# Performance work log

Measured on AMD Instinct MI355X. Metric: run time of the kernel, lower is better.

Reference implementation:

```python
import jax, jax.numpy as jnp
import numpy as np

N = 100_000
E = 1_600_000
F_IN = 128
HEADS = 8
OUT_H = 8   # per-head channels, concat -> 64
N_CLS = 40
K_HOPS = 10  # truncation order of heat-kernel Taylor series
NEG_SLOPE = 0.2
T_INIT = 5.0


def setup_inputs() -> dict:
    key = jax.random.key(0)
    ks = jax.random.split(key, 10)
    x = jax.random.normal(ks[0], (N, F_IN), jnp.float32)
    edge_index = jax.random.randint(ks[1], (2, E), 0, N, jnp.int32)
    t = jnp.full((F_IN,), T_INIT, jnp.float32)  # per-channel learnable diffusion time
    W1 = jax.random.normal(ks[2], (F_IN, HEADS * OUT_H), jnp.float32) / np.sqrt(F_IN).astype(np.float32)
    a_src1 = jax.random.normal(ks[3], (HEADS, OUT_H), jnp.float32) * 0.1
    a_dst1 = jax.random.normal(ks[4], (HEADS, OUT_H), jnp.float32) * 0.1
    b1 = jnp.zeros((HEADS * OUT_H,), jnp.float32)
    W2 = jax.random.normal(ks[5], (HEADS * OUT_H, N_CLS), jnp.float32) / np.sqrt(HEADS * OUT_H).astype(np.float32)
    a_src2 = jax.random.normal(ks[6], (1, N_CLS), jnp.float32) * 0.1
    a_dst2 = jax.random.normal(ks[7], (1, N_CLS), jnp.float32) * 0.1
    b2 = jnp.zeros((N_CLS,), jnp.float32)
    return {"x": x, "edge_index": edge_index, "t": t, "W1": W1, "a_src1": a_src1,
            "a_dst1": a_dst1, "b1": b1, "W2": W2, "a_src2": a_src2, "a_dst2": a_dst2, "b2": b2}


def _add_self_loops(edge_index, n):
    loop = jnp.arange(n, dtype=edge_index.dtype)
    return jnp.concatenate([edge_index, jnp.stack([loop, loop])], axis=1)


def _diffusion(x, src, dst, t, n):
    # heat kernel: exp(-t) * sum_k t^k/k! * A_hat^k x, per-channel t
    deg = jax.ops.segment_sum(jnp.ones_like(src, jnp.float32), dst, num_segments=n)
    dinv = jnp.where(deg > 0, jax.lax.rsqrt(jnp.maximum(deg, 1.0)), 0.0)
    norm = dinv[src] * dinv[dst]  # [E+N]

    def prop(h):
        return jax.ops.segment_sum(norm[:, None] * h[src], dst, num_segments=n)

    coef0 = jnp.exp(-t)  # [F]

    def step(carry, k):
        h, coef, acc = carry
        h = prop(h)
        coef = coef * t / k
        return (h, coef, acc + coef * h), None

    (_, _, out), _ = jax.lax.scan(step, (x, coef0, coef0 * x),
                                  jnp.arange(1, K_HOPS + 1, dtype=jnp.float32))
    return out


def _gat_layer(x, src, dst, W, a_s, a_d, b, heads, out_ch, concat, n):
    h = (x @ W).reshape(n, heads, out_ch)                  # [N,H,C]
    al_s = jnp.einsum('nhc,hc->nh', h, a_s)                # src attn logits
    al_d = jnp.einsum('nhc,hc->nh', h, a_d)
    e = jax.nn.leaky_relu(al_s[src] + al_d[dst], NEG_SLOPE)  # [E+N, H]
    emax = jax.ops.segment_max(e, dst, num_segments=n)       # stable softmax per target node
    ex = jnp.exp(e - emax[dst])
    denom = jax.ops.segment_sum(ex, dst, num_segments=n)
    alpha = ex / jnp.maximum(denom[dst], 1e-16)               # [E+N, H]
    out = jax.ops.segment_sum(alpha[:, :, None] * h[src], dst, num_segments=n)  # [N,H,C]
    out = out.reshape(n, heads * out_ch) if concat else out.mean(axis=1)
    return out + b


def reference(x, edge_index, t, W1, a_src1, a_dst1, b1, W2, a_src2, a_dst2, b2):
    n = x.shape[0]
    ei = _add_self_loops(edge_index, n)
    src, dst = ei[0], ei[1]
    h = _diffusion(x, src, dst, t, n)
    h = _gat_layer(h, src, dst, W1, a_src1, a_dst1, b1, HEADS, OUT_H, True, n)
    h = jax.nn.elu(h)
    h = _gat_layer(h, src, dst, W2, a_src2, a_dst2, b2, 1, N_CLS, False, n)
    return jax.nn.log_softmax(h, axis=1)
```

## Files before the change

kernel.cpp:

```cpp
#include <hip/hip_runtime.h>
#include <hip/hip_bf16.h>


static __device__ __forceinline__ unsigned pack_bf16x2(float a, float b) {
    __hip_bfloat162 p(__float2bfloat16(a), __float2bfloat16(b));
    return *reinterpret_cast<unsigned*>(&p);
}

__global__ void init_node_kernel(int* deg, int* cursor, int n) {
    int i = blockIdx.x * 256 + threadIdx.x;
    if (i < n) { deg[i] = 1; cursor[i] = 0; }
}

__global__ void edge_deg_kernel(const int* __restrict__ dst, int* deg, int E) {
    int e = blockIdx.x * 256 + threadIdx.x;
    if (e < E) atomicAdd(&deg[dst[e]], 1);
}

__global__ void alloc_kernel(const int* __restrict__ deg, float* dinv,
                             int* row_off, int* gcount, int n) {
    int i = blockIdx.x * 256 + threadIdx.x;
    if (i >= n) return;
    int dg = deg[i];
    dinv[i] = rsqrtf((float)dg);
    row_off[i] = atomicAdd(gcount, dg);
}

__global__ void scatter_kernel(const int* __restrict__ ei, const int* __restrict__ row_off,
                               int* cursor, const float* __restrict__ dinv,
                               int2* csr_pair, int E, int n) {
    int e = blockIdx.x * 256 + threadIdx.x;
    if (e >= E + n) return;
    int s, d;
    if (e < E) { s = ei[e]; d = ei[E + e]; } else { s = e - E; d = s; }
    int pos = atomicAdd(&cursor[d], 1);
    int slot = row_off[d] + pos;
    csr_pair[slot] = make_int2(s, __float_as_int(dinv[s] * dinv[d]));
}

__global__ void coef_kernel(const float* __restrict__ t, float* coefs) {
    int c = threadIdx.x;
    float tc = t[c];
    float v = expf(-tc);
    coefs[c] = v;
    for (int k = 1; k <= 10; ++k) { v *= tc / (float)k; coefs[k * 128 + c] = v; }
}

__global__ void init_diff_kernel(const float4* __restrict__ x4, const float* __restrict__ coefs,
                                 uint2* __restrict__ h, float4* __restrict__ acc4, int total4) {
    int i = blockIdx.x * 256 + threadIdx.x;
    if (i >= total4) return;
    float4 xv = x4[i];
    h[i] = make_uint2(pack_bf16x2(xv.x, xv.y), pack_bf16x2(xv.z, xv.w));
    const float4 c = *(const float4*)&coefs[(i & 31) * 4];
    acc4[i] = make_float4(c.x * xv.x, c.y * xv.y, c.z * xv.z, c.w * xv.w);
}

__global__ void hop_kernel(const int* __restrict__ row_off, const int* __restrict__ deg,
                           const int2* __restrict__ csr_pair,
                           const unsigned* __restrict__ h, unsigned* __restrict__ h_next,
                           float2* __restrict__ acc2, const float2* __restrict__ coefk2,
                           int n, int write_h) {
    int wid = (blockIdx.x << 2) + (threadIdx.x >> 6);
    int lane = threadIdx.x & 63;
    if (wid >= n) return;
    int off = row_off[wid];
    int cnt = deg[wid];
    float2 a0 = {0.f, 0.f}, a1 = {0.f, 0.f}, a2 = {0.f, 0.f}, a3 = {0.f, 0.f};
    for (int base = 0; base < cnt; base += 64) {
        int nb = min(64, cnt - base);
        int2 p = {0, 0};
        if (lane < nb) p = csr_pair[off + base + lane];
        int tt = 0;
        for (; tt + 3 < nb; tt += 4) {
            int s0 = __builtin_amdgcn_readlane(p.x, tt);
            int s1 = __builtin_amdgcn_readlane(p.x, tt + 1);
            int s2 = __builtin_amdgcn_readlane(p.x, tt + 2);
            int s3 = __builtin_amdgcn_readlane(p.x, tt + 3);
            float w0 = __int_as_float(__builtin_amdgcn_readlane(p.y, tt));
            float w1 = __int_as_float(__builtin_amdgcn_readlane(p.y, tt + 1));
            float w2 = __int_as_float(__builtin_amdgcn_readlane(p.y, tt + 2));
            float w3 = __int_as_float(__builtin_amdgcn_readlane(p.y, tt + 3));
            unsigned u0 = h[(size_t)s0 * 64 + lane];
            unsigned u1 = h[(size_t)s1 * 64 + lane];
            unsigned u2 = h[(size_t)s2 * 64 + lane];
            unsigned u3 = h[(size_t)s3 * 64 + lane];
            a0.x = fmaf(w0, __uint_as_float(u0 << 16), a0.x);
            a0.y = fmaf(w0, __uint_as_float(u0 & 0xffff0000u), a0.y);
            a1.x = fmaf(w1, __uint_as_float(u1 << 16), a1.x);
            a1.y = fmaf(w1, __uint_as_float(u1 & 0xffff0000u), a1.y);
            a2.x = fmaf(w2, __uint_as_float(u2 << 16), a2.x);
            a2.y = fmaf(w2, __uint_as_float(u2 & 0xffff0000u), a2.y);
            a3.x = fmaf(w3, __uint_as_float(u3 << 16), a3.x);
            a3.y = fmaf(w3, __uint_as_float(u3 & 0xffff0000u), a3.y);
        }
        for (; tt < nb; ++tt) {
            int s = __builtin_amdgcn_readlane(p.x, tt);
            float w = __int_as_float(__builtin_amdgcn_readlane(p.y, tt));
            unsigned u = h[(size_t)s * 64 + lane];
            a0.x = fmaf(w, __uint_as_float(u << 16), a0.x);
            a0.y = fmaf(w, __uint_as_float(u & 0xffff0000u), a0.y);
        }
    }
    float2 s;
    s.x = (a0.x + a1.x) + (a2.x + a3.x);
    s.y = (a0.y + a1.y) + (a2.y + a3.y);
    size_t o = (size_t)wid * 64 + lane;
    if (write_h) h_next[o] = pack_bf16x2(s.x, s.y);
    float2 c = coefk2[lane];
    float2 av = acc2[o];
    av.x = fmaf(c.x, s.x, av.x);
    av.y = fmaf(c.y, s.y, av.y);
    acc2[o] = av;
}

__global__ __launch_bounds__(256) void gemm1_kernel(
    const float* __restrict__ acc, const float* __restrict__ W1,
    const float* __restrict__ a_s, const float* __restrict__ a_d,
    float* __restrict__ h1, float* __restrict__ als, float* __restrict__ ald, int n) {
    __shared__ float Wl[128 * 64];
    __shared__ float Al[4][16 * 128];
    for (int i = threadIdx.x; i < 128 * 64; i += 256) Wl[i] = W1[i];
    int w = threadIdx.x >> 6;
    int lane = threadIdx.x & 63;
    int node0 = (blockIdx.x * 4 + w) * 16;
    const float4* accv4 = (const float4*)acc;
    float4* Av4 = (float4*)Al[w];
#pragma unroll
    for (int i = 0; i < 8; ++i) {
        int f4 = i * 64 + lane;
        int g4 = node0 * 32 + f4;
        float4 v = (g4 < n * 32) ? accv4[g4] : make_float4(0.f, 0.f, 0.f, 0.f);
        Av4[f4] = v;
    }
    __syncthreads();
    float sums[16];
#pragma unroll
    for (int nd = 0; nd < 16; ++nd) sums[nd] = 0.f;
#pragma unroll 1
    for (int kc = 0; kc < 16; ++kc) {
        float wr[8];
#pragma unroll
        for (int i = 0; i < 8; ++i) wr[i] = Wl[(kc * 8 + i) * 64 + lane];
#pragma unroll
        for (int nd = 0; nd < 16; ++nd) {
            float4 a = *(const float4*)&Al[w][nd * 128 + kc * 8];
            float4 b = *(const float4*)&Al[w][nd * 128 + kc * 8 + 4];
            float s = sums[nd];
            s = fmaf(wr[0], a.x, s); s = fmaf(wr[1], a.y, s);
            s = fmaf(wr[2], a.z, s); s = fmaf(wr[3], a.w, s);
            s = fmaf(wr[4], b.x, s); s = fmaf(wr[5], b.y, s);
            s = fmaf(wr[6], b.z, s); s = fmaf(wr[7], b.w, s);
            sums[nd] = s;
        }
    }
    float asv = a_s[lane], adv = a_d[lane];
#pragma unroll
    for (int nd = 0; nd < 16; ++nd) {
        int node = node0 + nd;
        if (node >= n) break;
        float sum = sums[nd];
        h1[(size_t)node * 64 + lane] = sum;
        float vs = sum * asv;
        float vd = sum * adv;
        vs += __shfl_xor(vs, 1); vs += __shfl_xor(vs, 2); vs += __shfl_xor(vs, 4);
        vd += __shfl_xor(vd, 1); vd += __shfl_xor(vd, 2); vd += __shfl_xor(vd, 4);
        if ((lane & 7) == 0) {
            als[(size_t)node * 8 + (lane >> 3)] = vs;
            ald[(size_t)node * 8 + (lane >> 3)] = vd;
        }
    }
}

__global__ void agg1_kernel(const int* __restrict__ row_off, const int* __restrict__ deg,
                            const int2* __restrict__ csr_pair,
                            const float* __restrict__ h1, const float* __restrict__ als,
                            const float* __restrict__ ald, const float* __restrict__ b1,
                            float* __restrict__ helu, int n) {
    int wid = (blockIdx.x << 2) + (threadIdx.x >> 6);
    int lane = threadIdx.x & 63;
    if (wid >= n) return;
    int head = lane >> 3;
    int off = row_off[wid];
    int cnt = deg[wid];
    float aldv = ald[(size_t)wid * 8 + head];
    float m = -1e30f, d = 0.f, accv = 0.f;
    for (int base = 0; base < cnt; base += 64) {
        int nb = min(64, cnt - base);
        int srcv = 0;
        if (lane < nb) srcv = csr_pair[off + base + lane].x;
        for (int tt = 0; tt < nb; ++tt) {
            int s = __builtin_amdgcn_readlane(srcv, tt);
            float e = als[(size_t)s * 8 + head] + aldv;
            e = e > 0.f ? e : 0.2f * e;
            float hv = h1[(size_t)s * 64 + lane];
            float mn = fmaxf(m, e);
            float scale = __expf(m - mn);
            float p = __expf(e - mn);
            d = fmaf(d, scale, p);
            accv = fmaf(accv, scale, p * hv);
            m = mn;
        }
    }
    float outv = accv / d + b1[lane];
    outv = outv > 0.f ? outv : expm1f(outv);
    helu[(size_t)wid * 64 + lane] = outv;
}

__global__ __launch_bounds__(256) void gemm2_kernel(
    const float* __restrict__ helu, const float* __restrict__ W2,
    const float* __restrict__ a_s, const float* __restrict__ a_d,
    float* __restrict__ h2, float* __restrict__ als, float* __restrict__ ald, int n) {
    __shared__ float Wl[64 * 40];
    __shared__ float Al[4][16 * 64];
    for (int i = threadIdx.x; i < 64 * 40; i += 256) Wl[i] = W2[i];
    int w = threadIdx.x >> 6;
    int lane = threadIdx.x & 63;
    int node0 = (blockIdx.x * 4 + w) * 16;
    const float4* hv4 = (const float4*)helu;
    float4* Av4 = (float4*)Al[w];
#pragma unroll
    for (int i = 0; i < 4; ++i) {
        int f4 = i * 64 + lane;
        int g4 = node0 * 16 + f4;
        float4 v = (g4 < n * 16) ? hv4[g4] : make_float4(0.f, 0.f, 0.f, 0.f);
        Av4[f4] = v;
    }
    __syncthreads();
    bool act = lane < 40;
    int li = act ? lane : 0;
    float sums[16];
#pragma unroll
    for (int nd = 0; nd < 16; ++nd) sums[nd] = 0.f;
#pragma unroll 1
    for (int kc = 0; kc < 8; ++kc) {
        float wr[8];
#pragma unroll
        for (int i = 0; i < 8; ++i) wr[i] = Wl[(kc * 8 + i) * 40 + li];
#pragma unroll
        for (int nd = 0; nd < 16; ++nd) {
            float4 a = *(const float4*)&Al[w][nd * 64 + kc * 8];
            float4 b = *(const float4*)&Al[w][nd * 64 + kc * 8 + 4];
            float s = sums[nd];
            s = fmaf(wr[0], a.x, s); s = fmaf(wr[1], a.y, s);
            s = fmaf(wr[2], a.z, s); s = fmaf(wr[3], a.w, s);
            s = fmaf(wr[4], b.x, s); s = fmaf(wr[5], b.y, s);
            s = fmaf(wr[6], b.z, s); s = fmaf(wr[7], b.w, s);
            sums[nd] = s;
        }
    }
    float asv = act ? a_s[lane] : 0.f;
    float adv = act ? a_d[lane] : 0.f;
#pragma unroll
    for (int nd = 0; nd < 16; ++nd) {
        int node = node0 + nd;
        if (node >= n) break;
        float sum = sums[nd];
        if (act) h2[(size_t)node * 40 + lane] = sum;
        float vs = act ? sum * asv : 0.f;
        float vd = act ? sum * adv : 0.f;
#pragma unroll
        for (int i = 32; i >= 1; i >>= 1) { vs += __shfl_xor(vs, i); vd += __shfl_xor(vd, i); }
        if (lane == 0) { als[node] = vs; ald[node] = vd; }
    }
}

__global__ void agg2_kernel(const int* __restrict__ row_off, const int* __restrict__ deg,
                            const int2* __restrict__ csr_pair,
                            const float* __restrict__ h2, const float* __restrict__ als,
                            const float* __restrict__ ald, const float* __restrict__ b2,
                            float* __restrict__ out, int n) {
    int wid = (blockIdx.x << 2) + (threadIdx.x >> 6);
    int lane = threadIdx.x & 63;
    if (wid >= n) return;
    bool act = lane < 40;
    int li = act ? lane : 0;
    int off = row_off[wid];
    int cnt = deg[wid];
    float aldv = ald[wid];
    float m = -1e30f, d = 0.f, accv = 0.f;
    for (int base = 0; base < cnt; base += 64) {
        int nb = min(64, cnt - base);
        int srcv = 0;
        if (lane < nb) srcv = csr_pair[off + base + lane].x;
        for (int tt = 0; tt < nb; ++tt) {
            int s = __builtin_amdgcn_readlane(srcv, tt);
            float e = als[s] + aldv;
            e = e > 0.f ? e : 0.2f * e;
            float hv = h2[(size_t)s * 40 + li];
            float mn = fmaxf(m, e);
            float scale = __expf(m - mn);
            float p = __expf(e - mn);
            d = fmaf(d, scale, p);
            accv = fmaf(accv, scale, p * hv);
            m = mn;
        }
    }
    float o = accv / d + (act ? b2[lane] : 0.f);
    float vv = act ? o : -1e30f;
#pragma unroll
    for (int i = 32; i >= 1; i >>= 1) vv = fmaxf(vv, __shfl_xor(vv, i));
    float ex = act ? __expf(o - vv) : 0.f;
#pragma unroll
    for (int i = 32; i >= 1; i >>= 1) ex += __shfl_xor(ex, i);
    if (act) out[(size_t)wid * 40 + lane] = o - vv - logf(ex);
}

extern "C" void kernel_launch(void* const* d_in, const int* in_sizes, int n_in,
                              void* d_out, int out_size, void* d_ws, size_t ws_size,
                              hipStream_t stream) {
    const float* x    = (const float*)d_in[0];
    const int*   ei   = (const int*)d_in[1];
    const float* t    = (const float*)d_in[2];
    const float* W1   = (const float*)d_in[3];
    const float* a_s1 = (const float*)d_in[4];
    const float* a_d1 = (const float*)d_in[5];
    const float* b1   = (const float*)d_in[6];
    const float* W2   = (const float*)d_in[7];
    const float* a_s2 = (const float*)d_in[8];
    const float* a_d2 = (const float*)d_in[9];
    const float* b2   = (const float*)d_in[10];
    float* out = (float*)d_out;

    const int N = in_sizes[0] / 128;
    const int E = in_sizes[1] / 2;

    char* w = (char*)d_ws;
    auto carve = [&](size_t bytes) {
        void* p = (void*)w;
        w += (bytes + 255) & ~(size_t)255;
        return p;
    };
    int*      deg      = (int*)carve((size_t)N * 4);
    int*      cursor   = (int*)carve((size_t)N * 4);
    int*      row_off  = (int*)carve((size_t)N * 4);
    int*      gcount   = (int*)carve(256);
    float*    dinv     = (float*)carve((size_t)N * 4);
    int2*     csr_pair = (int2*)carve((size_t)(E + N) * 8);
    float*    coefs    = (float*)carve(11 * 128 * 4);
    float*    als1     = (float*)carve((size_t)N * 8 * 4);
    float*    ald1     = (float*)carve((size_t)N * 8 * 4);
    float*    als2     = (float*)carve((size_t)N * 4);
    float*    ald2     = (float*)carve((size_t)N * 4);
    unsigned* hA       = (unsigned*)carve((size_t)N * 64 * 4);
    unsigned* hB       = (unsigned*)carve((size_t)N * 64 * 4);
    float*    acc      = (float*)carve((size_t)N * 128 * 4);
    float*    h1       = (float*)carve((size_t)N * 64 * 4);
    float*    helu     = (float*)carve((size_t)N * 64 * 4);
    float*    h2       = (float*)carve((size_t)N * 40 * 4);

    dim3 blk(256);
    int gN = (N + 255) / 256;
    int gE = (E + 255) / 256;
    int gEN = (E + N + 255) / 256;
    int gW = (N + 3) / 4;
    int gT = (N + 63) / 64;

    init_node_kernel<<<gN, blk, 0, stream>>>(deg, cursor, N);
    hipMemsetAsync(gcount, 0, 4, stream);
    edge_deg_kernel<<<gE, blk, 0, stream>>>(ei + E, deg, E);
    alloc_kernel<<<gN, blk, 0, stream>>>(deg, dinv, row_off, gcount, N);
    scatter_kernel<<<gEN, blk, 0, stream>>>(ei, row_off, cursor, dinv, csr_pair, E, N);
    coef_kernel<<<1, 128, 0, stream>>>(t, coefs);
    init_diff_kernel<<<(N * 32 + 255) / 256, blk, 0, stream>>>(
        (const float4*)x, coefs, (uint2*)hA, (float4*)acc, N * 32);

    unsigned* hc = hA;
    unsigned* hn = hB;
    for (int k = 1; k <= 10; ++k) {
        hop_kernel<<<gW, blk, 0, stream>>>(row_off, deg, csr_pair, hc, hn, (float2*)acc,
                                           (const float2*)(coefs + k * 128), N,
                                           k < 10 ? 1 : 0);
        unsigned* tmp = hc; hc = hn; hn = tmp;
    }

    gemm1_kernel<<<gT, blk, 0, stream>>>(acc, W1, a_s1, a_d1, h1, als1, ald1, N);
    agg1_kernel<<<gW, blk, 0, stream>>>(row_off, deg, csr_pair, h1, als1, ald1, b1, helu, N);
    gemm2_kernel<<<gT, blk, 0, stream>>>(helu, W2, a_s2, a_d2, h2, als2, ald2, N);
    agg2_kernel<<<gW, blk, 0, stream>>>(row_off, deg, csr_pair, h2, als2, ald2, b2, out, N);
}
```

Measured before the change: 1.410 ms.

## Store GAT features as bf16, pair edges per half-wave, drop online softmax max

```diff
diff --git a/kernel.cpp b/kernel.cpp
--- a/kernel.cpp
+++ b/kernel.cpp
@@ -72,19 +72,31 @@
         int2 p = {0, 0};
         if (lane < nb) p = csr_pair[off + base + lane];
         int tt = 0;
-        for (; tt + 3 < nb; tt += 4) {
+        for (; tt + 7 < nb; tt += 8) {
             int s0 = __builtin_amdgcn_readlane(p.x, tt);
             int s1 = __builtin_amdgcn_readlane(p.x, tt + 1);
             int s2 = __builtin_amdgcn_readlane(p.x, tt + 2);
             int s3 = __builtin_amdgcn_readlane(p.x, tt + 3);
+            int s4 = __builtin_amdgcn_readlane(p.x, tt + 4);
+            int s5 = __builtin_amdgcn_readlane(p.x, tt + 5);
+            int s6 = __builtin_amdgcn_readlane(p.x, tt + 6);
+            int s7 = __builtin_amdgcn_readlane(p.x, tt + 7);
             float w0 = __int_as_float(__builtin_amdgcn_readlane(p.y, tt));
             float w1 = __int_as_float(__builtin_amdgcn_readlane(p.y, tt + 1));
             float w2 = __int_as_float(__builtin_amdgcn_readlane(p.y, tt + 2));
             float w3 = __int_as_float(__builtin_amdgcn_readlane(p.y, tt + 3));
+            float w4 = __int_as_float(__builtin_amdgcn_readlane(p.y, tt + 4));
+            float w5 = __int_as_float(__builtin_amdgcn_readlane(p.y, tt + 5));
+            float w6 = __int_as_float(__builtin_amdgcn_readlane(p.y, tt + 6));
+            float w7 = __int_as_float(__builtin_amdgcn_readlane(p.y, tt + 7));
             unsigned u0 = h[(size_t)s0 * 64 + lane];
             unsigned u1 = h[(size_t)s1 * 64 + lane];
             unsigned u2 = h[(size_t)s2 * 64 + lane];
             unsigned u3 = h[(size_t)s3 * 64 + lane];
+            unsigned u4 = h[(size_t)s4 * 64 + lane];
+            unsigned u5 = h[(size_t)s5 * 64 + lane];
+            unsigned u6 = h[(size_t)s6 * 64 + lane];
+            unsigned u7 = h[(size_t)s7 * 64 + lane];
             a0.x = fmaf(w0, __uint_as_float(u0 << 16), a0.x);
             a0.y = fmaf(w0, __uint_as_float(u0 & 0xffff0000u), a0.y);
             a1.x = fmaf(w1, __uint_as_float(u1 << 16), a1.x);
@@ -93,6 +105,14 @@
             a2.y = fmaf(w2, __uint_as_float(u2 & 0xffff0000u), a2.y);
             a3.x = fmaf(w3, __uint_as_float(u3 << 16), a3.x);
             a3.y = fmaf(w3, __uint_as_float(u3 & 0xffff0000u), a3.y);
+            a0.x = fmaf(w4, __uint_as_float(u4 << 16), a0.x);
+            a0.y = fmaf(w4, __uint_as_float(u4 & 0xffff0000u), a0.y);
+            a1.x = fmaf(w5, __uint_as_float(u5 << 16), a1.x);
+            a1.y = fmaf(w5, __uint_as_float(u5 & 0xffff0000u), a1.y);
+            a2.x = fmaf(w6, __uint_as_float(u6 << 16), a2.x);
+            a2.y = fmaf(w6, __uint_as_float(u6 & 0xffff0000u), a2.y);
+            a3.x = fmaf(w7, __uint_as_float(u7 << 16), a3.x);
+            a3.y = fmaf(w7, __uint_as_float(u7 & 0xffff0000u), a3.y);
         }
         for (; tt < nb; ++tt) {
             int s = __builtin_amdgcn_readlane(p.x, tt);
@@ -117,7 +137,7 @@
 __global__ __launch_bounds__(256) void gemm1_kernel(
     const float* __restrict__ acc, const float* __restrict__ W1,
     const float* __restrict__ a_s, const float* __restrict__ a_d,
-    float* __restrict__ h1, float* __restrict__ als, float* __restrict__ ald, int n) {
+    unsigned* __restrict__ h1b, float* __restrict__ als, float* __restrict__ ald, int n) {
     __shared__ float Wl[128 * 64];
     __shared__ float Al[4][16 * 128];
     for (int i = threadIdx.x; i < 128 * 64; i += 256) Wl[i] = W1[i];
@@ -160,7 +180,8 @@
         int node = node0 + nd;
         if (node >= n) break;
         float sum = sums[nd];
-        h1[(size_t)node * 64 + lane] = sum;
+        float partner = __shfl_xor(sum, 1);
+        if ((lane & 1) == 0) h1b[(size_t)node * 32 + (lane >> 1)] = pack_bf16x2(sum, partner);
         float vs = sum * asv;
         float vd = sum * adv;
         vs += __shfl_xor(vs, 1); vs += __shfl_xor(vs, 2); vs += __shfl_xor(vs, 4);
@@ -174,43 +195,80 @@
 
 __global__ void agg1_kernel(const int* __restrict__ row_off, const int* __restrict__ deg,
                             const int2* __restrict__ csr_pair,
-                            const float* __restrict__ h1, const float* __restrict__ als,
+                            const unsigned* __restrict__ h1b, const float* __restrict__ als,
                             const float* __restrict__ ald, const float* __restrict__ b1,
-                            float* __restrict__ helu, int n) {
+                            float2* __restrict__ helu2, int n) {
     int wid = (blockIdx.x << 2) + (threadIdx.x >> 6);
     int lane = threadIdx.x & 63;
     if (wid >= n) return;
-    int head = lane >> 3;
+    int half = lane >> 5;
+    int l = lane & 31;
+    int head = l >> 2;
     int off = row_off[wid];
     int cnt = deg[wid];
     float aldv = ald[(size_t)wid * 8 + head];
-    float m = -1e30f, d = 0.f, accv = 0.f;
+    float dA = 0.f, dB = 0.f;
+    float2 aA = {0.f, 0.f}, aB = {0.f, 0.f};
     for (int base = 0; base < cnt; base += 64) {
         int nb = min(64, cnt - base);
         int srcv = 0;
         if (lane < nb) srcv = csr_pair[off + base + lane].x;
-        for (int tt = 0; tt < nb; ++tt) {
-            int s = __builtin_amdgcn_readlane(srcv, tt);
-            float e = als[(size_t)s * 8 + head] + aldv;
+        int j = 0;
+        for (; j + 3 < nb; j += 4) {
+            int sA0 = __builtin_amdgcn_readlane(srcv, j);
+            int sA1 = __builtin_amdgcn_readlane(srcv, j + 1);
+            int sB0 = __builtin_amdgcn_readlane(srcv, j + 2);
+            int sB1 = __builtin_amdgcn_readlane(srcv, j + 3);
+            int sA = half ? sA1 : sA0;
+            int sB = half ? sB1 : sB0;
+            float eA = als[(size_t)sA * 8 + head] + aldv;
+            float eB = als[(size_t)sB * 8 + head] + aldv;
+            eA = eA > 0.f ? eA : 0.2f * eA;
+            eB = eB > 0.f ? eB : 0.2f * eB;
+            float pA = __expf(eA);
+            float pB = __expf(eB);
+            unsigned uA = h1b[(size_t)sA * 32 + l];
+            unsigned uB = h1b[(size_t)sB * 32 + l];
+            dA += pA; dB += pB;
+            aA.x = fmaf(pA, __uint_as_float(uA << 16), aA.x);
+            aA.y = fmaf(pA, __uint_as_float(uA & 0xffff0000u), aA.y);
+            aB.x = fmaf(pB, __uint_as_float(uB << 16), aB.x);
+            aB.y = fmaf(pB, __uint_as_float(uB & 0xffff0000u), aB.y);
+        }
+        for (; j < nb; j += 2) {
+            int s0 = __builtin_amdgcn_readlane(srcv, j);
+            int s1 = (j + 1 < nb) ? __builtin_amdgcn_readlane(srcv, j + 1) : -1;
+            int s = half ? s1 : s0;
+            bool valid = s >= 0;
+            int ss = valid ? s : 0;
+            float e = als[(size_t)ss * 8 + head] + aldv;
             e = e > 0.f ? e : 0.2f * e;
-            float hv = h1[(size_t)s * 64 + lane];
-            float mn = fmaxf(m, e);
-            float scale = __expf(m - mn);
-            float p = __expf(e - mn);
-            d = fmaf(d, scale, p);
-            accv = fmaf(accv, scale, p * hv);
-            m = mn;
-        }
-    }
-    float outv = accv / d + b1[lane];
-    outv = outv > 0.f ? outv : expm1f(outv);
-    helu[(size_t)wid * 64 + lane] = outv;
+            float p = valid ? __expf(e) : 0.f;
+            unsigned u = h1b[(size_t)ss * 32 + l];
+            dA += p;
+            aA.x = fmaf(p, __uint_as_float(u << 16), aA.x);
+            aA.y = fmaf(p, __uint_as_float(u & 0xffff0000u), aA.y);
+        }
+    }
+    float d = dA + dB;
+    float2 accv = make_float2(aA.x + aB.x, aA.y + aB.y);
+    d += __shfl_xor(d, 32);
+    accv.x += __shfl_xor(accv.x, 32);
+    accv.y += __shfl_xor(accv.y, 32);
+    if (half == 0) {
+        float inv = 1.f / d;
+        float ox = fmaf(accv.x, inv, b1[2 * l]);
+        float oy = fmaf(accv.y, inv, b1[2 * l + 1]);
+        ox = ox > 0.f ? ox : expm1f(ox);
+        oy = oy > 0.f ? oy : expm1f(oy);
+        helu2[(size_t)wid * 32 + l] = make_float2(ox, oy);
+    }
 }
 
 __global__ __launch_bounds__(256) void gemm2_kernel(
     const float* __restrict__ helu, const float* __restrict__ W2,
     const float* __restrict__ a_s, const float* __restrict__ a_d,
-    float* __restrict__ h2, float* __restrict__ als, float* __restrict__ ald, int n) {
+    unsigned* __restrict__ h2b, float* __restrict__ als, float* __restrict__ ald, int n) {
     __shared__ float Wl[64 * 40];
     __shared__ float Al[4][16 * 64];
     for (int i = threadIdx.x; i < 64 * 40; i += 256) Wl[i] = W2[i];
@@ -256,7 +314,8 @@
         int node = node0 + nd;
         if (node >= n) break;
         float sum = sums[nd];
-        if (act) h2[(size_t)node * 40 + lane] = sum;
+        float partner = __shfl_xor(sum, 1);
+        if (act && (lane & 1) == 0) h2b[(size_t)node * 20 + (lane >> 1)] = pack_bf16x2(sum, partner);
         float vs = act ? sum * asv : 0.f;
         float vd = act ? sum * adv : 0.f;
 #pragma unroll
@@ -267,43 +326,81 @@
 
 __global__ void agg2_kernel(const int* __restrict__ row_off, const int* __restrict__ deg,
                             const int2* __restrict__ csr_pair,
-                            const float* __restrict__ h2, const float* __restrict__ als,
+                            const unsigned* __restrict__ h2b, const float* __restrict__ als,
                             const float* __restrict__ ald, const float* __restrict__ b2,
                             float* __restrict__ out, int n) {
     int wid = (blockIdx.x << 2) + (threadIdx.x >> 6);
     int lane = threadIdx.x & 63;
     if (wid >= n) return;
-    bool act = lane < 40;
-    int li = act ? lane : 0;
+    int half = lane >> 5;
+    int l = lane & 31;
+    bool act = l < 20;
+    int li = act ? l : 0;
     int off = row_off[wid];
     int cnt = deg[wid];
     float aldv = ald[wid];
-    float m = -1e30f, d = 0.f, accv = 0.f;
+    float dA = 0.f, dB = 0.f;
+    float2 aA = {0.f, 0.f}, aB = {0.f, 0.f};
     for (int base = 0; base < cnt; base += 64) {
         int nb = min(64, cnt - base);
         int srcv = 0;
         if (lane < nb) srcv = csr_pair[off + base + lane].x;
-        for (int tt = 0; tt < nb; ++tt) {
-            int s = __builtin_amdgcn_readlane(srcv, tt);
-            float e = als[s] + aldv;
+        int j = 0;
+        for (; j + 3 < nb; j += 4) {
+            int sA0 = __builtin_amdgcn_readlane(srcv, j);
+            int sA1 = __builtin_amdgcn_readlane(srcv, j + 1);
+            int sB0 = __builtin_amdgcn_readlane(srcv, j + 2);
+            int sB1 = __builtin_amdgcn_readlane(srcv, j + 3);
+            int sA = half ? sA1 : sA0;
+            int sB = half ? sB1 : sB0;
+            float eA = als[sA] + aldv;
+            float eB = als[sB] + aldv;
+            eA = eA > 0.f ? eA : 0.2f * eA;
+            eB = eB > 0.f ? eB : 0.2f * eB;
+            float pA = __expf(eA);
+            float pB = __expf(eB);
+            unsigned uA = h2b[(size_t)sA * 20 + li];
+            unsigned uB = h2b[(size_t)sB * 20 + li];
+            dA += pA; dB += pB;
+            aA.x = fmaf(pA, __uint_as_float(uA << 16), aA.x);
+            aA.y = fmaf(pA, __uint_as_float(uA & 0xffff0000u), aA.y);
+            aB.x = fmaf(pB, __uint_as_float(uB << 16), aB.x);
+            aB.y = fmaf(pB, __uint_as_float(uB & 0xffff0000u), aB.y);
+        }
+        for (; j < nb; j += 2) {
+            int s0 = __builtin_amdgcn_readlane(srcv, j);
+            int s1 = (j + 1 < nb) ? __builtin_amdgcn_readlane(srcv, j + 1) : -1;
+            int s = half ? s1 : s0;
+            bool valid = s >= 0;
+            int ss = valid ? s : 0;
+            float e = als[ss] + aldv;
             e = e > 0.f ? e : 0.2f * e;
-            float hv = h2[(size_t)s * 40 + li];
-            float mn = fmaxf(m, e);
-            float scale = __expf(m - mn);
-            float p = __expf(e - mn);
-            d = fmaf(d, scale, p);
-            accv = fmaf(accv, scale, p * hv);
-            m = mn;
-        }
-    }
-    float o = accv / d + (act ? b2[lane] : 0.f);
-    float vv = act ? o : -1e30f;
-#pragma unroll
-    for (int i = 32; i >= 1; i >>= 1) vv = fmaxf(vv, __shfl_xor(vv, i));
-    float ex = act ? __expf(o - vv) : 0.f;
-#pragma unroll
-    for (int i = 32; i >= 1; i >>= 1) ex += __shfl_xor(ex, i);
-    if (act) out[(size_t)wid * 40 + lane] = o - vv - logf(ex);
+            float p = valid ? __expf(e) : 0.f;
+            unsigned u = h2b[(size_t)ss * 20 + li];
+            dA += p;
+            aA.x = fmaf(p, __uint_as_float(u << 16), aA.x);
+            aA.y = fmaf(p, __uint_as_float(u & 0xffff0000u), aA.y);
+        }
+    }
+    float d = dA + dB;
+    float2 accv = make_float2(aA.x + aB.x, aA.y + aB.y);
+    d += __shfl_xor(d, 32);
+    accv.x += __shfl_xor(accv.x, 32);
+    accv.y += __shfl_xor(accv.y, 32);
+    float inv = 1.f / d;
+    bool live = (half == 0) && act;
+    float ox = live ? fmaf(accv.x, inv, b2[2 * l]) : -1e30f;
+    float oy = live ? fmaf(accv.y, inv, b2[2 * l + 1]) : -1e30f;
+    float vv = fmaxf(ox, oy);
+#pragma unroll
+    for (int i = 16; i >= 1; i >>= 1) vv = fmaxf(vv, __shfl_xor(vv, i));
+    float ex = live ? (__expf(ox - vv) + __expf(oy - vv)) : 0.f;
+#pragma unroll
+    for (int i = 16; i >= 1; i >>= 1) ex += __shfl_xor(ex, i);
+    if (live) {
+        float lse = vv + logf(ex);
+        *(float2*)&out[(size_t)wid * 40 + 2 * l] = make_float2(ox - lse, oy - lse);
+    }
 }
 
 extern "C" void kernel_launch(void* const* d_in, const int* in_sizes, int n_in,
@@ -345,9 +442,9 @@
     unsigned* hA       = (unsigned*)carve((size_t)N * 64 * 4);
     unsigned* hB       = (unsigned*)carve((size_t)N * 64 * 4);
     float*    acc      = (float*)carve((size_t)N * 128 * 4);
-    float*    h1       = (float*)carve((size_t)N * 64 * 4);
+    unsigned* h1b      = (unsigned*)carve((size_t)N * 32 * 4);
     float*    helu     = (float*)carve((size_t)N * 64 * 4);
-    float*    h2       = (float*)carve((size_t)N * 40 * 4);
+    unsigned* h2b      = (unsigned*)carve((size_t)N * 20 * 4);
 
     dim3 blk(256);
     int gN = (N + 255) / 256;
@@ -374,8 +471,9 @@
         unsigned* tmp = hc; hc = hn; hn = tmp;
     }
 
-    gemm1_kernel<<<gT, blk, 0, stream>>>(acc, W1, a_s1, a_d1, h1, als1, ald1, N);
-    agg1_kernel<<<gW, blk, 0, stream>>>(row_off, deg, csr_pair, h1, als1, ald1, b1, helu, N);
-    gemm2_kernel<<<gT, blk, 0, stream>>>(helu, W2, a_s2, a_d2, h2, als2, ald2, N);
-    agg2_kernel<<<gW, blk, 0, stream>>>(row_off, deg, csr_pair, h2, als2, ald2, b2, out, N);
-}
+    gemm1_kernel<<<gT, blk, 0, stream>>>(acc, W1, a_s1, a_d1, h1b, als1, ald1, N);
+    agg1_kernel<<<gW, blk, 0, stream>>>(row_off, deg, csr_pair, h1b, als1, ald1, b1,
+                                        (float2*)helu, N);
+    gemm2_kernel<<<gT, blk, 0, stream>>>(helu, W2, a_s2, a_d2, h2b, als2, ald2, N);
+    agg2_kernel<<<gW, blk, 0, stream>>>(row_off, deg, csr_pair, h2b, als2, ald2, b2, out, N);
+}
```

Result: faster. 1.311 ms (-7.0%).
